# Kernel optimization log

Hardware: AMD Instinct MI355X
Metric: run time of the kernel (lower is better)

## Reference

```python
import jax, jax.numpy as jnp
import numpy as np

B, T, H, L = 32, 2048, 256, 2  # batch, seq_len, hidden(=input), num_layers


def setup_inputs() -> dict:
    key = jax.random.key(0)
    k1, k2, k3 = jax.random.split(key, 3)
    x = jax.random.normal(k1, (B, T, H), dtype=jnp.float32)
    # Stacked per-layer gate weights: order (i, f, o, c_hat), Linear acts on concat([inp, h])
    bound = 1.0 / np.sqrt(2 * H)
    W = jax.random.uniform(k2, (L, 4, H, 2 * H), dtype=jnp.float32, minval=-bound, maxval=bound)
    b = jax.random.uniform(k3, (L, 4, H), dtype=jnp.float32, minval=-bound, maxval=bound)
    return {"x": x, "W": W, "b": b}


def reference(x, W, b):
    Bsz, Tlen, _ = x.shape
    nlayers, _, Hdim, _ = W.shape

    def step(carry, x_t):
        h, c = carry  # each [L, B, H]
        inp = x_t     # [B, H]
        hs, cs = [], []
        for l in range(nlayers):
            comb = jnp.concatenate([inp, h[l]], axis=-1)          # [B, 2H]
            gates = jnp.einsum('bi,ghi->bgh', comb, W[l]) + b[l]  # [B, 4, H]
            i_g = jax.nn.sigmoid(gates[:, 0])
            f_g = jax.nn.sigmoid(gates[:, 1])
            o_g = jax.nn.sigmoid(gates[:, 2])
            c_hat = jnp.tanh(gates[:, 3])
            c_new = f_g * c[l] + i_g * c_hat
            h_new = o_g * jnp.tanh(c_new)
            hs.append(h_new)
            cs.append(c_new)
            inp = h_new
        return (jnp.stack(hs), jnp.stack(cs)), inp

    h0 = jnp.zeros((nlayers, Bsz, Hdim), dtype=x.dtype)
    c0 = jnp.zeros((nlayers, Bsz, Hdim), dtype=x.dtype)
    (hT, cT), outs = jax.lax.scan(step, (h0, c0), jnp.swapaxes(x, 0, 1))
    outputs = jnp.swapaxes(outs, 0, 1)  # [B, T, H]
    return outputs, (hT[-1], cT[-1])
```

## Files before the change

kernel.cpp:

```cpp
#include <hip/hip_runtime.h>

#define BB 32
#define TT 2048
#define HH 256
#define NT 512

typedef unsigned long long ull;
typedef unsigned int uint;

__device__ __forceinline__ float sigm(float v) { return 1.0f / (1.0f + __expf(-v)); }

__device__ __forceinline__ int aload(const int* p) {
  return __hip_atomic_load(p, __ATOMIC_RELAXED, __HIP_MEMORY_SCOPE_AGENT);
}
__device__ __forceinline__ void astore(int* p, int v) {
  __hip_atomic_store(p, v, __ATOMIC_RELAXED, __HIP_MEMORY_SCOPE_AGENT);
}
__device__ __forceinline__ ull aload64(const ull* p) {
  return __hip_atomic_load(p, __ATOMIC_RELAXED, __HIP_MEMORY_SCOPE_AGENT);
}
__device__ __forceinline__ void astore64(ull* p, ull v) {
  __hip_atomic_store(p, v, __ATOMIC_RELAXED, __HIP_MEMORY_SCOPE_AGENT);
}

__global__ __launch_bounds__(NT) void lstm_scan(
    const float* __restrict__ x,
    const float* __restrict__ W,
    const float* __restrict__ bias,
    float* __restrict__ out,
    ull* __restrict__ ring,
    int* __restrict__ sync)
{
    const int bid   = blockIdx.x;
    const int c     = bid & 7;
    const int ug    = bid >> 3;
    const int layer = c >> 2;
    const int grp   = c & 3;
    const int tid   = threadIdx.x;
    const int lane  = tid & 63;
    const int wave  = tid >> 6;
    const int ks    = lane & 15;
    const int gh    = (lane >> 4) & 1;
    const int bh    = lane >> 5;
    const int col   = ug * 8 + wave;
    const int rb    = bh * 4;

    int* mOwn = sync + c * 32;
    int* mSib = sync + (4 + grp) * 32;
    ull* ringOwn = ring + (size_t)c * 8192;
    ull* ringIn  = ring + (size_t)grp * 8192;

    __shared__ float inp[2][8][268];
    __shared__ float hrec[2][8][268];

    float4 wA[8], wB[8];
    const float* WAp = W + (((size_t)layer * 4 + gh * 2)     * HH + col) * (2 * HH);
    const float* WBp = W + (((size_t)layer * 4 + gh * 2 + 1) * HH + col) * (2 * HH);
    #pragma unroll
    for (int j = 0; j < 8; ++j) {
        wA[j] = *(const float4*)(WAp + j * 64 + ks * 4);
        wB[j] = *(const float4*)(WBp + j * 64 + ks * 4);
    }

    float bb[4];
    #pragma unroll
    for (int g = 0; g < 4; ++g) bb[g] = bias[((size_t)layer * 4 + g) * HH + col];

    const int srow = tid >> 8;
    const int scol = tid & 255;

    float xr0 = 0.f, xr1 = 0.f, xr2 = 0.f, xr3 = 0.f;
    if (layer == 0) {
        const float* xb = x + (size_t)(grp * 8 + srow) * TT * HH + scol;
        xr0 = xb[0 * 2 * TT * HH];
        xr1 = xb[1 * 2 * TT * HH];
        xr2 = xb[2 * 2 * TT * HH];
        xr3 = xb[3 * 2 * TT * HH];
    }

    float c_state = 0.f;

    for (int t = 0; t < TT; ++t) {
        const int p = t & 1;
        int gv = 0x7fffffff;
        if (tid < 32)                    gv = aload(&mOwn[tid]);
        else if (layer == 0 && tid < 64) gv = aload(&mSib[tid - 32]);

        if (layer == 0) {
            inp[p][srow + 0][scol] = xr0;
            inp[p][srow + 2][scol] = xr1;
            inp[p][srow + 4][scol] = xr2;
            inp[p][srow + 6][scol] = xr3;
            const int tn = (t + 1 < TT) ? t + 1 : t;
            const float* xb = x + ((size_t)(grp * 8 + srow) * TT + tn) * HH + scol;
            xr0 = xb[0 * 2 * TT * HH];
            xr1 = xb[1 * 2 * TT * HH];
            xr2 = xb[2 * 2 * TT * HH];
            xr3 = xb[3 * 2 * TT * HH];
        } else {
            const ull* rin = ringIn + (t & 3) * 2048;
            const uint want = (uint)(t + 1);
            uint pend = 0xFu; ull v[4]; int tries = 0;
            for (;;) {
                #pragma unroll
                for (int j = 0; j < 4; ++j)
                    if (pend & (1u << j)) v[j] = aload64(&rin[tid + 512 * j]);
                #pragma unroll
                for (int j = 0; j < 4; ++j)
                    if ((pend & (1u << j)) && (uint)v[j] == want) {
                        inp[p][srow + 2 * j][scol] = __uint_as_float((uint)(v[j] >> 32));
                        pend &= ~(1u << j);
                    }
                if (!pend) break;
                if (++tries > 4) __builtin_amdgcn_s_sleep(1);
            }
        }
        __syncthreads();

        float aA0 = 0.f, aA1 = 0.f, aA2 = 0.f, aA3 = 0.f;
        float aB0 = 0.f, aB1 = 0.f, aB2 = 0.f, aB3 = 0.f;
        #pragma unroll
        for (int j = 0; j < 4; ++j) {
            const int kof = j * 64 + ks * 4;
            float4 w0 = wA[j], w1 = wB[j];
            float4 v0 = *(const float4*)&inp[p][rb + 0][kof];
            float4 v1 = *(const float4*)&inp[p][rb + 1][kof];
            float4 v2 = *(const float4*)&inp[p][rb + 2][kof];
            float4 v3 = *(const float4*)&inp[p][rb + 3][kof];
            aA0 += v0.x * w0.x + v0.y * w0.y + v0.z * w0.z + v0.w * w0.w;
            aB0 += v0.x * w1.x + v0.y * w1.y + v0.z * w1.z + v0.w * w1.w;
            aA1 += v1.x * w0.x + v1.y * w0.y + v1.z * w0.z + v1.w * w0.w;
            aB1 += v1.x * w1.x + v1.y * w1.y + v1.z * w1.z + v1.w * w1.w;
            aA2 += v2.x * w0.x + v2.y * w0.y + v2.z * w0.z + v2.w * w0.w;
            aB2 += v2.x * w1.x + v2.y * w1.y + v2.z * w1.z + v2.w * w1.w;
            aA3 += v3.x * w0.x + v3.y * w0.y + v3.z * w0.z + v3.w * w0.w;
            aB3 += v3.x * w1.x + v3.y * w1.y + v3.z * w1.z + v3.w * w1.w;
        }

        {
            const ull* rr_ = ringOwn + ((t + 3) & 3) * 2048;
            const uint want = (uint)t;
            uint pend = 0xFu; ull v[4]; int tries = 0;
            for (;;) {
                #pragma unroll
                for (int j = 0; j < 4; ++j)
                    if (pend & (1u << j)) v[j] = aload64(&rr_[tid + 512 * j]);
                #pragma unroll
                for (int j = 0; j < 4; ++j)
                    if ((pend & (1u << j)) && (uint)v[j] == want) {
                        hrec[p][srow + 2 * j][scol] = __uint_as_float((uint)(v[j] >> 32));
                        pend &= ~(1u << j);
                    }
                if (!pend) break;
                if (++tries > 4) __builtin_amdgcn_s_sleep(1);
            }
        }
        if (tid < 32) {
            while (gv < t - 2) { __builtin_amdgcn_s_sleep(1); gv = aload(&mOwn[tid]); }
        } else if (layer == 0 && tid < 64) {
            while (gv < t - 3) { __builtin_amdgcn_s_sleep(1); gv = aload(&mSib[tid - 32]); }
        }
        __syncthreads();
        if (tid == 0) astore(&mOwn[ug], t + 1);

        #pragma unroll
        for (int j = 4; j < 8; ++j) {
            const int kof = (j - 4) * 64 + ks * 4;
            float4 w0 = wA[j], w1 = wB[j];
            float4 v0 = *(const float4*)&hrec[p][rb + 0][kof];
            float4 v1 = *(const float4*)&hrec[p][rb + 1][kof];
            float4 v2 = *(const float4*)&hrec[p][rb + 2][kof];
            float4 v3 = *(const float4*)&hrec[p][rb + 3][kof];
            aA0 += v0.x * w0.x + v0.y * w0.y + v0.z * w0.z + v0.w * w0.w;
            aB0 += v0.x * w1.x + v0.y * w1.y + v0.z * w1.z + v0.w * w1.w;
            aA1 += v1.x * w0.x + v1.y * w0.y + v1.z * w0.z + v1.w * w0.w;
            aB1 += v1.x * w1.x + v1.y * w1.y + v1.z * w1.z + v1.w * w1.w;
            aA2 += v2.x * w0.x + v2.y * w0.y + v2.z * w0.z + v2.w * w0.w;
            aB2 += v2.x * w1.x + v2.y * w1.y + v2.z * w1.z + v2.w * w1.w;
            aA3 += v3.x * w0.x + v3.y * w0.y + v3.z * w0.z + v3.w * w0.w;
            aB3 += v3.x * w1.x + v3.y * w1.y + v3.z * w1.z + v3.w * w1.w;
        }

        #pragma unroll
        for (int m = 1; m <= 8; m <<= 1) {
            aA0 += __shfl_xor(aA0, m);
            aA1 += __shfl_xor(aA1, m);
            aA2 += __shfl_xor(aA2, m);
            aA3 += __shfl_xor(aA3, m);
            aB0 += __shfl_xor(aB0, m);
            aB1 += __shfl_xor(aB1, m);
            aB2 += __shfl_xor(aB2, m);
            aB3 += __shfl_xor(aB3, m);
        }
        float oA0 = __shfl_xor(aA0, 16), oA1 = __shfl_xor(aA1, 16);
        float oA2 = __shfl_xor(aA2, 16), oA3 = __shfl_xor(aA3, 16);
        float qB0 = __shfl_xor(aB0, 16), qB1 = __shfl_xor(aB1, 16);
        float qB2 = __shfl_xor(aB2, 16), qB3 = __shfl_xor(aB3, 16);

        if (gh == 0 && ks < 4) {
            const int bl = rb + ks;
            float iv = ks == 0 ? aA0 : ks == 1 ? aA1 : ks == 2 ? aA2 : aA3;
            float fv = ks == 0 ? aB0 : ks == 1 ? aB1 : ks == 2 ? aB2 : aB3;
            float ov = ks == 0 ? oA0 : ks == 1 ? oA1 : ks == 2 ? oA2 : oA3;
            float qv = ks == 0 ? qB0 : ks == 1 ? qB1 : ks == 2 ? qB2 : qB3;
            float ig = sigm(iv + bb[0]);
            float fg = sigm(fv + bb[1]);
            float og = sigm(ov + bb[2]);
            float ch = tanhf(qv + bb[3]);
            c_state = fg * c_state + ig * ch;
            float hn = og * tanhf(c_state);
            astore64(&ringOwn[(t & 3) * 2048 + bl * 256 + col],
                     ((ull)__float_as_uint(hn) << 32) | (ull)(uint)(t + 1));
            if (layer == 1) {
                const int bglob = grp * 8 + bl;
                out[((size_t)bglob * TT + t) * HH + col] = hn;
                if (t == TT - 1) {
                    float* tail = out + (size_t)BB * TT * HH;
                    tail[bglob * HH + col] = hn;
                    tail[BB * HH + bglob * HH + col] = c_state;
                }
            }
        }
    }
}

extern "C" void kernel_launch(void* const* d_in, const int* in_sizes, int n_in,
                              void* d_out, int out_size, void* d_ws, size_t ws_size,
                              hipStream_t stream) {
    (void)in_sizes; (void)n_in; (void)out_size; (void)ws_size;
    const float* x    = (const float*)d_in[0];
    const float* W    = (const float*)d_in[1];
    const float* bias = (const float*)d_in[2];
    float* out  = (float*)d_out;
    int*   sync = (int*)d_ws;
    ull*   ring = (ull*)((char*)d_ws + 4096);

    hipMemsetAsync(d_ws, 0, 4096 + 8 * 8192 * sizeof(ull), stream);
    hipLaunchKernelGGL(lstm_scan, dim3(256), dim3(NT), 0, stream, x, W, bias, out, ring, sync);
}
```

Before: 6.401 ms.

## Repartition LSTM blocks into 8 batch groups of 4 rows with 16 columns each

Changes the work split across the 256 blocks from 4 batch groups of 8 rows to 8 batch groups of 4 rows. Each block now owns 16 hidden columns (two per wave, one per 32-lane half) instead of 8. This shrinks the ring buffers, the shared staging and the per-step global polling volume per block, and halves the number of peer blocks each group waits on. The cost is that each block loads weights for more columns, and there are more independent sync groups and flag sets.

```diff
diff --git a/kernel.cpp b/kernel.cpp
--- a/kernel.cpp
+++ b/kernel.cpp
@@ -32,26 +32,25 @@
     int* __restrict__ sync)
 {
     const int bid   = blockIdx.x;
-    const int c     = bid & 7;
-    const int ug    = bid >> 3;
-    const int layer = c >> 2;
-    const int grp   = c & 3;
+    const int grp   = bid & 7;
+    const int layer = (bid >> 3) & 1;
+    const int ug    = bid >> 4;
+    const int c     = layer * 8 + grp;
     const int tid   = threadIdx.x;
     const int lane  = tid & 63;
     const int wave  = tid >> 6;
     const int ks    = lane & 15;
     const int gh    = (lane >> 4) & 1;
-    const int bh    = lane >> 5;
-    const int col   = ug * 8 + wave;
-    const int rb    = bh * 4;
-
-    int* mOwn = sync + c * 32;
-    int* mSib = sync + (4 + grp) * 32;
-    ull* ringOwn = ring + (size_t)c * 8192;
-    ull* ringIn  = ring + (size_t)grp * 8192;
-
-    __shared__ float inp[2][8][268];
-    __shared__ float hrec[2][8][268];
+    const int cp    = lane >> 5;
+    const int col   = ug * 16 + wave * 2 + cp;
+
+    int* mOwn = sync + c * 16;
+    int* mSib = sync + (8 + grp) * 16;
+    ull* ringOwn = ring + (size_t)c * 4096;
+    ull* ringIn  = ring + (size_t)grp * 4096;
+
+    __shared__ float inp[2][4][260];
+    __shared__ float hrec[2][4][260];
 
     float4 wA[8], wB[8];
     const float* WAp = W + (((size_t)layer * 4 + gh * 2)     * HH + col) * (2 * HH);
@@ -69,13 +68,11 @@
     const int srow = tid >> 8;
     const int scol = tid & 255;
 
-    float xr0 = 0.f, xr1 = 0.f, xr2 = 0.f, xr3 = 0.f;
+    float xr0 = 0.f, xr1 = 0.f;
     if (layer == 0) {
-        const float* xb = x + (size_t)(grp * 8 + srow) * TT * HH + scol;
-        xr0 = xb[0 * 2 * TT * HH];
-        xr1 = xb[1 * 2 * TT * HH];
-        xr2 = xb[2 * 2 * TT * HH];
-        xr3 = xb[3 * 2 * TT * HH];
+        const float* xb = x + (size_t)(grp * 4 + srow) * TT * HH + scol;
+        xr0 = xb[0];
+        xr1 = xb[2 * TT * HH];
     }
 
     float c_state = 0.f;
@@ -83,34 +80,31 @@
     for (int t = 0; t < TT; ++t) {
         const int p = t & 1;
         int gv = 0x7fffffff;
-        if (tid < 32)                    gv = aload(&mOwn[tid]);
-        else if (layer == 0 && tid < 64) gv = aload(&mSib[tid - 32]);
+        if (tid < 16)                    gv = aload(&mOwn[tid]);
+        else if (layer == 0 && tid < 48) { if (tid >= 32) gv = aload(&mSib[tid - 32]); }
 
         if (layer == 0) {
             inp[p][srow + 0][scol] = xr0;
             inp[p][srow + 2][scol] = xr1;
-            inp[p][srow + 4][scol] = xr2;
-            inp[p][srow + 6][scol] = xr3;
             const int tn = (t + 1 < TT) ? t + 1 : t;
-            const float* xb = x + ((size_t)(grp * 8 + srow) * TT + tn) * HH + scol;
-            xr0 = xb[0 * 2 * TT * HH];
-            xr1 = xb[1 * 2 * TT * HH];
-            xr2 = xb[2 * 2 * TT * HH];
-            xr3 = xb[3 * 2 * TT * HH];
+            const float* xb = x + ((size_t)(grp * 4 + srow) * TT + tn) * HH + scol;
+            xr0 = xb[0];
+            xr1 = xb[2 * TT * HH];
         } else {
-            const ull* rin = ringIn + (t & 3) * 2048;
+            const ull* rin = ringIn + (t & 3) * 1024;
             const uint want = (uint)(t + 1);
-            uint pend = 0xFu; ull v[4]; int tries = 0;
+            uint pend = 0x3u; ull v0, v1; int tries = 0;
             for (;;) {
-                #pragma unroll
-                for (int j = 0; j < 4; ++j)
-                    if (pend & (1u << j)) v[j] = aload64(&rin[tid + 512 * j]);
-                #pragma unroll
-                for (int j = 0; j < 4; ++j)
-                    if ((pend & (1u << j)) && (uint)v[j] == want) {
-                        inp[p][srow + 2 * j][scol] = __uint_as_float((uint)(v[j] >> 32));
-                        pend &= ~(1u << j);
-                    }
+                if (pend & 1u) v0 = aload64(&rin[tid]);
+                if (pend & 2u) v1 = aload64(&rin[tid + 512]);
+                if ((pend & 1u) && (uint)v0 == want) {
+                    inp[p][srow][scol] = __uint_as_float((uint)(v0 >> 32));
+                    pend &= ~1u;
+                }
+                if ((pend & 2u) && (uint)v1 == want) {
+                    inp[p][srow + 2][scol] = __uint_as_float((uint)(v1 >> 32));
+                    pend &= ~2u;
+                }
                 if (!pend) break;
                 if (++tries > 4) __builtin_amdgcn_s_sleep(1);
             }
@@ -123,10 +117,10 @@
         for (int j = 0; j < 4; ++j) {
             const int kof = j * 64 + ks * 4;
             float4 w0 = wA[j], w1 = wB[j];
-            float4 v0 = *(const float4*)&inp[p][rb + 0][kof];
-            float4 v1 = *(const float4*)&inp[p][rb + 1][kof];
-            float4 v2 = *(const float4*)&inp[p][rb + 2][kof];
-            float4 v3 = *(const float4*)&inp[p][rb + 3][kof];
+            float4 v0 = *(const float4*)&inp[p][0][kof];
+            float4 v1 = *(const float4*)&inp[p][1][kof];
+            float4 v2 = *(const float4*)&inp[p][2][kof];
+            float4 v3 = *(const float4*)&inp[p][3][kof];
             aA0 += v0.x * w0.x + v0.y * w0.y + v0.z * w0.z + v0.w * w0.w;
             aB0 += v0.x * w1.x + v0.y * w1.y + v0.z * w1.z + v0.w * w1.w;
             aA1 += v1.x * w0.x + v1.y * w0.y + v1.z * w0.z + v1.w * w0.w;
@@ -138,26 +132,27 @@
         }
 
         {
-            const ull* rr_ = ringOwn + ((t + 3) & 3) * 2048;
+            const ull* rr_ = ringOwn + ((t + 3) & 3) * 1024;
             const uint want = (uint)t;
-            uint pend = 0xFu; ull v[4]; int tries = 0;
+            uint pend = 0x3u; ull v0, v1; int tries = 0;
             for (;;) {
-                #pragma unroll
-                for (int j = 0; j < 4; ++j)
-                    if (pend & (1u << j)) v[j] = aload64(&rr_[tid + 512 * j]);
-                #pragma unroll
-                for (int j = 0; j < 4; ++j)
-                    if ((pend & (1u << j)) && (uint)v[j] == want) {
-                        hrec[p][srow + 2 * j][scol] = __uint_as_float((uint)(v[j] >> 32));
-                        pend &= ~(1u << j);
-                    }
+                if (pend & 1u) v0 = aload64(&rr_[tid]);
+                if (pend & 2u) v1 = aload64(&rr_[tid + 512]);
+                if ((pend & 1u) && (uint)v0 == want) {
+                    hrec[p][srow][scol] = __uint_as_float((uint)(v0 >> 32));
+                    pend &= ~1u;
+                }
+                if ((pend & 2u) && (uint)v1 == want) {
+                    hrec[p][srow + 2][scol] = __uint_as_float((uint)(v1 >> 32));
+                    pend &= ~2u;
+                }
                 if (!pend) break;
                 if (++tries > 4) __builtin_amdgcn_s_sleep(1);
             }
         }
-        if (tid < 32) {
+        if (tid < 16) {
             while (gv < t - 2) { __builtin_amdgcn_s_sleep(1); gv = aload(&mOwn[tid]); }
-        } else if (layer == 0 && tid < 64) {
+        } else if (layer == 0 && tid >= 32 && tid < 48) {
             while (gv < t - 3) { __builtin_amdgcn_s_sleep(1); gv = aload(&mSib[tid - 32]); }
         }
         __syncthreads();
@@ -167,10 +162,10 @@
         for (int j = 4; j < 8; ++j) {
             const int kof = (j - 4) * 64 + ks * 4;
             float4 w0 = wA[j], w1 = wB[j];
-            float4 v0 = *(const float4*)&hrec[p][rb + 0][kof];
-            float4 v1 = *(const float4*)&hrec[p][rb + 1][kof];
-            float4 v2 = *(const float4*)&hrec[p][rb + 2][kof];
-            float4 v3 = *(const float4*)&hrec[p][rb + 3][kof];
+            float4 v0 = *(const float4*)&hrec[p][0][kof];
+            float4 v1 = *(const float4*)&hrec[p][1][kof];
+            float4 v2 = *(const float4*)&hrec[p][2][kof];
+            float4 v3 = *(const float4*)&hrec[p][3][kof];
             aA0 += v0.x * w0.x + v0.y * w0.y + v0.z * w0.z + v0.w * w0.w;
             aB0 += v0.x * w1.x + v0.y * w1.y + v0.z * w1.z + v0.w * w1.w;
             aA1 += v1.x * w0.x + v1.y * w0.y + v1.z * w0.z + v1.w * w0.w;
@@ -198,7 +193,7 @@
         float qB2 = __shfl_xor(aB2, 16), qB3 = __shfl_xor(aB3, 16);
 
         if (gh == 0 && ks < 4) {
-            const int bl = rb + ks;
+            const int bl = ks;
             float iv = ks == 0 ? aA0 : ks == 1 ? aA1 : ks == 2 ? aA2 : aA3;
             float fv = ks == 0 ? aB0 : ks == 1 ? aB1 : ks == 2 ? aB2 : aB3;
             float ov = ks == 0 ? oA0 : ks == 1 ? oA1 : ks == 2 ? oA2 : oA3;
@@ -209,10 +204,10 @@
             float ch = tanhf(qv + bb[3]);
             c_state = fg * c_state + ig * ch;
             float hn = og * tanhf(c_state);
-            astore64(&ringOwn[(t & 3) * 2048 + bl * 256 + col],
+            astore64(&ringOwn[(t & 3) * 1024 + bl * 256 + col],
                      ((ull)__float_as_uint(hn) << 32) | (ull)(uint)(t + 1));
             if (layer == 1) {
-                const int bglob = grp * 8 + bl;
+                const int bglob = grp * 4 + bl;
                 out[((size_t)bglob * TT + t) * HH + col] = hn;
                 if (t == TT - 1) {
                     float* tail = out + (size_t)BB * TT * HH;
@@ -235,6 +230,6 @@
     int*   sync = (int*)d_ws;
     ull*   ring = (ull*)((char*)d_ws + 4096);
 
-    hipMemsetAsync(d_ws, 0, 4096 + 8 * 8192 * sizeof(ull), stream);
+    hipMemsetAsync(d_ws, 0, 4096 + 16 * 4096 * sizeof(ull), stream);
     hipLaunchKernelGGL(lstm_scan, dim3(256), dim3(NT), 0, stream, x, W, bias, out, ring, sync);
 }
```

Result: faster. 5.913 ms (-7.6%).
